# Kernel tuning notes

Hardware: AMD Instinct MI355X
Metric: run time of the kernel (lower is better)

## Reference

```python
import jax, jax.numpy as jnp
import numpy as np

LOG2PI = float(np.log(2.0 * np.pi))


def setup_inputs() -> dict:
    key = jax.random.key(0)
    ks = jax.random.split(key, 5)
    B, T, XD, C = 128, 2050, 6, 64
    return {
        "x": jax.random.normal(ks[0], (B, T, XD), jnp.float32),
        "observation_means": jax.random.uniform(ks[1], (C, XD), dtype=jnp.float32),
        "observation_stddevs": jax.random.uniform(ks[2], (C, XD), dtype=jnp.float32),
        "log_A": jax.random.normal(ks[3], (C, C), jnp.float32),
        "log_pi": jax.random.normal(ks[4], (C,), jnp.float32),
    }


def _emission_logprob(x, means, stds):
    # Normal(means[:, :4], relu(stds[:, :4]) + 0.1).log_prob(x[:, :, :4]) summed over feat dim
    mu = means[:, :4]                       # (C,4)
    sigma = jax.nn.relu(stds[:, :4]) + 0.1  # (C,4)
    z = (x[:, :, None, :4] - mu) / sigma    # (B,T,C,4)
    return jnp.sum(-0.5 * z * z - jnp.log(sigma) - 0.5 * LOG2PI, axis=-1)  # (B,T,C)


def _forward_scalers(logp, log_A, log_pi):
    # scaled HMM forward pass; returns per-step log normalizers (T,B)
    a0 = logp[:, 0] + log_pi
    s0 = jax.nn.logsumexp(a0, axis=-1)
    a0n = a0 - s0[:, None]

    def step(a_prev, lp_t):
        a = lp_t + jax.nn.logsumexp(a_prev[:, :, None] + log_A[None], axis=1)
        s = jax.nn.logsumexp(a, axis=-1)
        return a - s[:, None], s

    _, s_rest = jax.lax.scan(step, a0n, jnp.swapaxes(logp[:, 1:], 0, 1))
    return jnp.concatenate([s0[None], s_rest], axis=0)  # (T,B)


def _viterbi(logp, log_A, log_pi):
    d0 = logp[:, 0] + log_pi  # (B,C)

    def step(d_prev, lp_t):
        scores = d_prev[:, :, None] + log_A[None]  # (B,C_prev,C_cur)
        psi_t = jnp.argmax(scores, axis=1)
        d = jnp.max(scores, axis=1) + lp_t
        return d, psi_t

    d_last, psi = jax.lax.scan(step, d0, jnp.swapaxes(logp[:, 1:], 0, 1))  # psi: (T-1,B,C)
    c_last = jnp.argmax(d_last, axis=-1)  # (B,)

    def back(c_next, psi_t):
        c_t = jnp.take_along_axis(psi_t, c_next[:, None], axis=1)[:, 0]
        return c_t, c_t

    _, cs = jax.lax.scan(back, c_last, psi, reverse=True)  # (T-1,B)
    c = jnp.concatenate([cs, c_last[None]], axis=0)  # (T,B)
    return jnp.swapaxes(c, 0, 1)  # (B,T)


def reference(x, observation_means, observation_stddevs, log_A, log_pi):
    logA = jax.nn.log_softmax(log_A, axis=1)
    logpi = jax.nn.log_softmax(log_pi, axis=0)
    logp = _emission_logprob(x, observation_means, observation_stddevs)  # (B,T,C)
    scalers = _forward_scalers(logp, logA, logpi)                         # (T,B)
    logp_x = jnp.sum(scalers, axis=0)                                     # (B,)
    c_est = _viterbi(logp, logA, logpi)                                   # (B,T) int
    return logp_x, c_est
```

## Files before the change

### kernel.cpp

```cpp
#include <hip/hip_runtime.h>

#define T_LEN 2050
#define B_SZ 128
#define NCHUNK 33
#define HL2PI 0.91893853320467274178f

__device__ __forceinline__ float waveMax(float v) {
#pragma unroll
    for (int off = 32; off >= 1; off >>= 1)
        v = fmaxf(v, __shfl_xor(v, off, 64));
    return v;
}
__device__ __forceinline__ float waveSum(float v) {
#pragma unroll
    for (int off = 32; off >= 1; off >>= 1)
        v += __shfl_xor(v, off, 64);
    return v;
}
__device__ __forceinline__ void waveArgmax(float& v, int& idx) {
#pragma unroll
    for (int off = 32; off >= 1; off >>= 1) {
        float ov = __shfl_xor(v, off, 64);
        int   oi = __shfl_xor(idx, off, 64);
        if (ov > v || (ov == v && oi < idx)) { v = ov; idx = oi; }
    }
}
__device__ __forceinline__ void cfence() { asm volatile("" ::: "memory"); }

__device__ __forceinline__ float dppSumAll(float v) {
#define SSTEP(ctrl) { int t_ = __builtin_amdgcn_update_dpp(0, __float_as_int(v), ctrl, 0xf, 0xf, true); \
                      v = v + __int_as_float(t_); }
    SSTEP(0x111) SSTEP(0x112) SSTEP(0x114) SSTEP(0x118) SSTEP(0x142) SSTEP(0x143)
#undef SSTEP
    return __int_as_float(__builtin_amdgcn_readlane(__float_as_int(v), 63));
}
__device__ __forceinline__ float dppMaxAll(float v) {
#define MSTEP(ctrl) { int t_ = __builtin_amdgcn_update_dpp(__float_as_int(v), __float_as_int(v), ctrl, 0xf, 0xf, false); \
                      v = fmaxf(v, __int_as_float(t_)); }
    MSTEP(0x111) MSTEP(0x112) MSTEP(0x114) MSTEP(0x118) MSTEP(0x142) MSTEP(0x143)
#undef MSTEP
    return __int_as_float(__builtin_amdgcn_readlane(__float_as_int(v), 63));
}
__device__ __forceinline__ float rlane(int bits, int lane) {
    return __int_as_float(__builtin_amdgcn_readlane(bits, lane));
}

extern "C" __global__ __launch_bounds__(64, 1)
void hmm_prep(const float* __restrict__ logA_in,
              const float* __restrict__ logpi_in,
              float* __restrict__ lAg,
              float* __restrict__ lpig)
{
    __shared__ float la[64 * 65];
    __shared__ float rowlse[64];
    const int j = threadIdx.x;
#pragma unroll
    for (int k = 0; k < 64; ++k)
        la[k * 65 + j] = logA_in[k * 64 + j];
    cfence();
    {
        float m = -1e30f;
#pragma unroll
        for (int k = 0; k < 64; ++k) m = fmaxf(m, la[j * 65 + k]);
        float s = 0.f;
#pragma unroll
        for (int k = 0; k < 64; ++k) s += expf(la[j * 65 + k] - m);
        rowlse[j] = m + logf(s);
    }
    cfence();
    {
        float v = logpi_in[j];
        float m = waveMax(v);
        float s = waveSum(expf(v - m));
        lpig[j] = v - (m + logf(s));
    }
    float4* o = (float4*)lAg;
#pragma unroll
    for (int k = 0; k < 16; ++k) {
        float4 v;
        v.x = la[(4 * k + 0) * 65 + j] - rowlse[4 * k + 0];
        v.y = la[(4 * k + 1) * 65 + j] - rowlse[4 * k + 1];
        v.z = la[(4 * k + 2) * 65 + j] - rowlse[4 * k + 2];
        v.w = la[(4 * k + 3) * 65 + j] - rowlse[4 * k + 3];
        o[j * 16 + k] = v;
    }
}

extern "C" __global__ __launch_bounds__(256)
void hmm_emis(const float* __restrict__ x,
              const float* __restrict__ means,
              const float* __restrict__ stds,
              float* __restrict__ buf)
{
    const int wid = blockIdx.x * 4 + (threadIdx.x >> 6);
    const int j = threadIdx.x & 63;
    const int t = wid >> 7;
    const int b = wid & 127;

    const float* xt = x + ((size_t)b * T_LEN + t) * 6;
    float x0 = xt[0], x1 = xt[1], x2 = xt[2], x3 = xt[3];

    float mu0 = means[j * 6 + 0], mu1 = means[j * 6 + 1];
    float mu2 = means[j * 6 + 2], mu3 = means[j * 6 + 3];
    float sg0 = fmaxf(stds[j * 6 + 0], 0.f) + 0.1f;
    float sg1 = fmaxf(stds[j * 6 + 1], 0.f) + 0.1f;
    float sg2 = fmaxf(stds[j * 6 + 2], 0.f) + 0.1f;
    float sg3 = fmaxf(stds[j * 6 + 3], 0.f) + 0.1f;
    float ls0 = logf(sg0), ls1 = logf(sg1), ls2 = logf(sg2), ls3 = logf(sg3);

    float z0 = (x0 - mu0) / sg0, z1 = (x1 - mu1) / sg1;
    float z2 = (x2 - mu2) / sg2, z3 = (x3 - mu3) / sg3;
    float e0 = ((-0.5f * z0) * z0 - ls0) - HL2PI;
    float e1 = ((-0.5f * z1) * z1 - ls1) - HL2PI;
    float e2 = ((-0.5f * z2) * z2 - ls2) - HL2PI;
    float e3 = ((-0.5f * z3) * z3 - ls3) - HL2PI;
    float lp = ((e0 + e1) + e2) + e3;

    buf[((size_t)b * T_LEN + t) * 64 + j] = lp;
}

extern "C" __global__ __launch_bounds__(64, 1)
void hmm_main(const float* __restrict__ x,
              const float* __restrict__ means,
              const float* __restrict__ stds,
              const float* __restrict__ lAg,
              const float* __restrict__ lpig,
              float* __restrict__ out,
              float* __restrict__ buf,
              int* __restrict__ c_last)
{
    __shared__ __align__(16) float xs[12304];

    const int j   = threadIdx.x;
    const int bid = blockIdx.x;
    const bool is_fwd = (bid < B_SZ);
    const int b = is_fwd ? bid : bid - B_SZ;

    float lpi = lpig[j];

    if (is_fwd) {
        {
            const float4* xg4 = (const float4*)(x + (size_t)b * T_LEN * 6);
            float4* xs4 = (float4*)xs;
            for (int i = j; i < 3075; i += 64) xs4[i] = xg4[i];
        }
        float mu0 = means[j * 6 + 0], mu1 = means[j * 6 + 1];
        float mu2 = means[j * 6 + 2], mu3 = means[j * 6 + 3];
        float sg0 = fmaxf(stds[j * 6 + 0], 0.f) + 0.1f;
        float sg1 = fmaxf(stds[j * 6 + 1], 0.f) + 0.1f;
        float sg2 = fmaxf(stds[j * 6 + 2], 0.f) + 0.1f;
        float sg3 = fmaxf(stds[j * 6 + 3], 0.f) + 0.1f;
        float ls0 = logf(sg0), ls1 = logf(sg1), ls2 = logf(sg2), ls3 = logf(sg3);
        float i0 = 1.f / sg0, i1 = 1.f / sg1, i2 = 1.f / sg2, i3 = 1.f / sg3;
        float cst = -(ls0 + ls1 + ls2 + ls3) - 4.f * HL2PI;

        float Ac[64];
        {
            const float4* g = (const float4*)lAg;
#pragma unroll
            for (int k = 0; k < 16; ++k) {
                float4 v = g[j * 16 + k];
                Ac[4 * k + 0] = __expf(v.x); Ac[4 * k + 1] = __expf(v.y);
                Ac[4 * k + 2] = __expf(v.z); Ac[4 * k + 3] = __expf(v.w);
            }
        }
        cfence();

        float z0 = (xs[0] - mu0) * i0, z1 = (xs[1] - mu1) * i1;
        float z2 = (xs[2] - mu2) * i2, z3 = (xs[3] - mu3) * i3;
        float a0 = (cst - 0.5f * (z0 * z0 + z1 * z1 + z2 * z2 + z3 * z3)) + lpi;
        float m0a = dppMaxAll(a0);
        float u = __expf(a0 - m0a);
        float s0 = dppSumAll(u);
        double acc = (double)(m0a + __logf(s0));
        u *= (1.0f / s0);

        float mm_c, e_c;
        {
            float y0 = (xs[6] - mu0) * i0, y1 = (xs[7] - mu1) * i1;
            float y2 = (xs[8] - mu2) * i2, y3 = (xs[9] - mu3) * i3;
            float lp1 = cst - 0.5f * (y0 * y0 + y1 * y1 + y2 * y2 + y3 * y3);
            mm_c = dppMaxAll(lp1);
            e_c  = __expf(lp1 - mm_c);
        }

#pragma unroll 1
        for (int t = 1; t < T_LEN; ++t) {
            int o = ((t + 1 < T_LEN) ? (t + 1) : t) * 6;
            float y0 = xs[o], y1 = xs[o + 1], y2 = xs[o + 2], y3 = xs[o + 3];

            int ub = __float_as_int(u);
            float q0 = 0.f, q1 = 0.f, q2 = 0.f, q3 = 0.f;
#pragma unroll
            for (int k = 0; k < 16; ++k) {
                q0 = fmaf(rlane(ub, 4 * k + 0), Ac[4 * k + 0], q0);
                q1 = fmaf(rlane(ub, 4 * k + 1), Ac[4 * k + 1], q1);
                q2 = fmaf(rlane(ub, 4 * k + 2), Ac[4 * k + 2], q2);
                q3 = fmaf(rlane(ub, 4 * k + 3), Ac[4 * k + 3], q3);
            }
            float q = (q0 + q1) + (q2 + q3);
            u = q * e_c;
            acc += (double)mm_c;
            if ((t & 3) == 0) {
                float ss = dppSumAll(u);
                acc += (double)__logf(ss);
                u *= (1.0f / ss);
            }

            float w0 = (y0 - mu0) * i0, w1 = (y1 - mu1) * i1;
            float w2 = (y2 - mu2) * i2, w3 = (y3 - mu3) * i3;
            float lpn = cst - 0.5f * (w0 * w0 + w1 * w1 + w2 * w2 + w3 * w3);
            float mmn = dppMaxAll(lpn);
            e_c  = __expf(lpn - mmn);
            mm_c = mmn;
        }
        float sf = dppSumAll(u);
        acc += (double)__logf(sf);
        if (j == 0) out[b] = (float)acc;
    } else {
        float lA[64];
        {
            const float4* g = (const float4*)lAg;
#pragma unroll
            for (int k = 0; k < 16; ++k) {
                float4 v = g[j * 16 + k];
                lA[4 * k + 0] = v.x; lA[4 * k + 1] = v.y;
                lA[4 * k + 2] = v.z; lA[4 * k + 3] = v.w;
            }
        }
        float* bb = buf + (size_t)b * T_LEN * 64 + j;

        float dn = bb[0] + lpi;
        float l0 = bb[64], l1 = bb[128], l2 = bb[192], l3 = bb[256];
        bb[0] = dn;

#pragma unroll 1
        for (int t = 1; t < T_LEN; ++t) {
            float lp_c = l0; l0 = l1; l1 = l2; l2 = l3;
            int tp = t + 4; if (tp > T_LEN - 1) tp = T_LEN - 1;
            l3 = bb[(size_t)tp * 64];

            int db = __float_as_int(dn);
            float m0 = -3.4e38f, m1 = -3.4e38f, m2 = -3.4e38f, m3 = -3.4e38f;
#pragma unroll
            for (int k = 0; k < 8; ++k) {
                float t0 = rlane(db, 8 * k + 0) + lA[8 * k + 0];
                float t1 = rlane(db, 8 * k + 1) + lA[8 * k + 1];
                float t2 = rlane(db, 8 * k + 2) + lA[8 * k + 2];
                float t3 = rlane(db, 8 * k + 3) + lA[8 * k + 3];
                float t4 = rlane(db, 8 * k + 4) + lA[8 * k + 4];
                float t5 = rlane(db, 8 * k + 5) + lA[8 * k + 5];
                float t6 = rlane(db, 8 * k + 6) + lA[8 * k + 6];
                float t7 = rlane(db, 8 * k + 7) + lA[8 * k + 7];
                m0 = fmaxf(fmaxf(m0, t0), t1);
                m1 = fmaxf(fmaxf(m1, t2), t3);
                m2 = fmaxf(fmaxf(m2, t4), t5);
                m3 = fmaxf(fmaxf(m3, t6), t7);
            }
            float best = fmaxf(fmaxf(m0, m1), fmaxf(m2, m3));
            dn = best + lp_c;
            bb[(size_t)t * 64] = dn;
        }

        float vv = dn; int idx = j;
        waveArgmax(vv, idx);
        if (j == 0) c_last[b] = idx;
    }
}

extern "C" __global__ __launch_bounds__(256)
void hmm_psi(const float* __restrict__ buf,
             const float* __restrict__ lAg,
             unsigned char* __restrict__ psi)
{
    __shared__ __align__(16) float sd[4][64];
    const int warp = threadIdx.x >> 6;
    const int j = threadIdx.x & 63;
    const int wid = blockIdx.x * 4 + warp;

    float lA[64];
    {
        const float4* g = (const float4*)lAg;
#pragma unroll
        for (int k = 0; k < 16; ++k) {
            float4 v = g[j * 16 + k];
            lA[4 * k + 0] = v.x; lA[4 * k + 1] = v.y;
            lA[4 * k + 2] = v.z; lA[4 * k + 3] = v.w;
        }
    }
    const float4* dv = (const float4*)sd[warp];
    const int NP = 2049 * B_SZ;

    for (int p = wid; p < NP; p += 8192) {
        const int t = (p >> 7) + 1;
        const int b = p & 127;
        float dval = buf[((size_t)b * T_LEN + (t - 1)) * 64 + j];
        sd[warp][j] = dval;

        float bv0 = -3.4e38f, bv1 = -3.4e38f, bv2 = -3.4e38f, bv3 = -3.4e38f;
        int bi0 = 0, bi1 = 1, bi2 = 2, bi3 = 3;
#pragma unroll
        for (int k = 0; k < 16; ++k) {
            float4 dd = dv[k];
            float v0 = dd.x + lA[4 * k + 0];
            float v1 = dd.y + lA[4 * k + 1];
            float v2 = dd.z + lA[4 * k + 2];
            float v3 = dd.w + lA[4 * k + 3];
            if (v0 > bv0) { bv0 = v0; bi0 = 4 * k + 0; }
            if (v1 > bv1) { bv1 = v1; bi1 = 4 * k + 1; }
            if (v2 > bv2) { bv2 = v2; bi2 = 4 * k + 2; }
            if (v3 > bv3) { bv3 = v3; bi3 = 4 * k + 3; }
        }
        float best = bv0; int bidx = bi0;
        if (bv1 > best || (bv1 == best && bi1 < bidx)) { best = bv1; bidx = bi1; }
        if (bv2 > best || (bv2 == best && bi2 < bidx)) { best = bv2; bidx = bi2; }
        if (bv3 > best || (bv3 == best && bi3 < bidx)) { best = bv3; bidx = bi3; }

        psi[((size_t)t * B_SZ + b) * 64 + j] = (unsigned char)bidx;
    }
}

extern "C" __global__ __launch_bounds__(256)
void hmm_compose(const unsigned char* __restrict__ psi,
                 unsigned char* __restrict__ mt)
{
    const int w = blockIdx.x * 4 + (threadIdx.x >> 6);
    const int j = threadIdx.x & 63;
    const int g = w % NCHUNK;
    const int b = w / NCHUNK;
    const int e = (g < NCHUNK - 1) ? g * 64 + 64 : (T_LEN - 1);
    int M = j;
    for (int t = e; t >= g * 64 + 1; --t)
        M = psi[((size_t)t * B_SZ + b) * 64 + M];
    mt[((size_t)g * B_SZ + b) * 64 + j] = (unsigned char)M;
}

extern "C" __global__ __launch_bounds__(64, 1)
void hmm_fill(const unsigned char* __restrict__ psi,
              const unsigned char* __restrict__ mt,
              const int* __restrict__ c_last,
              float* __restrict__ out)
{
    __shared__ int sb[NCHUNK];
    const int b = blockIdx.x;
    const int g = threadIdx.x;
    const int cl = c_last[b];
    if (g == 0) {
        int cur = cl;
        for (int q = NCHUNK - 1; q >= 0; --q) {
            cur = mt[((size_t)q * B_SZ + b) * 64 + cur];
            sb[q] = cur;
        }
    }
    cfence();
    float* oc = out + B_SZ + (size_t)b * T_LEN;
    if (g == NCHUNK) {
        oc[T_LEN - 1] = (float)cl;
    } else if (g < NCHUNK) {
        const int e = (g < NCHUNK - 1) ? g * 64 + 64 : (T_LEN - 1);
        int s = (g < NCHUNK - 1) ? sb[g + 1] : cl;
        for (int t = e; t >= g * 64 + 1; --t) {
            s = psi[((size_t)t * B_SZ + b) * 64 + s];
            oc[t - 1] = (float)s;
        }
    }
}

extern "C" void kernel_launch(void* const* d_in, const int* in_sizes, int n_in,
                              void* d_out, int out_size, void* d_ws, size_t ws_size,
                              hipStream_t stream)
{
    const float* x      = (const float*)d_in[0];
    const float* means  = (const float*)d_in[1];
    const float* stds   = (const float*)d_in[2];
    const float* logA   = (const float*)d_in[3];
    const float* logpi  = (const float*)d_in[4];
    float* out = (float*)d_out;

    char* base = (char*)d_ws;
    float*         buf  = (float*)base;
    unsigned char* psi  = (unsigned char*)(base + 67174400);
    unsigned char* mt   = (unsigned char*)(base + 83968000);
    int*           cl   = (int*)(base + 84238336);
    float*         lAg  = (float*)(base + 84238848);
    float*         lpig = (float*)(base + 84255232);

    hipLaunchKernelGGL(hmm_prep, dim3(1), dim3(64), 0, stream, logA, logpi, lAg, lpig);
    hipLaunchKernelGGL(hmm_emis, dim3((T_LEN * B_SZ) / 4), dim3(256), 0, stream,
                       x, means, stds, buf);
    hipLaunchKernelGGL(hmm_main, dim3(2 * B_SZ), dim3(64), 0, stream,
                       x, means, stds, lAg, lpig, out, buf, cl);
    hipLaunchKernelGGL(hmm_psi, dim3(2048), dim3(256), 0, stream, buf, lAg, psi);
    hipLaunchKernelGGL(hmm_compose, dim3((NCHUNK * B_SZ) / 4), dim3(256), 0, stream, psi, mt);
    hipLaunchKernelGGL(hmm_fill, dim3(B_SZ), dim3(64), 0, stream, psi, mt, cl, out);
}
```

Before: 1.059 ms.

## Process two batch sequences per wavefront in forward and Viterbi recurrences

Each hmm_main block now handles two batch elements, interleaving their independent recurrences so the lane-broadcast/FMA or max chains of one sequence can hide the latency of the other. The grid halves from 256 to 128 single-wave blocks, and shared memory doubles to hold both x sequences. This trades per-wave ILP for fewer concurrent waves and higher register pressure, on a GPU with far more CUs than blocks.

```diff
diff --git a/kernel.cpp b/kernel.cpp
--- a/kernel.cpp
+++ b/kernel.cpp
@@ -129,20 +129,23 @@
               float* __restrict__ buf,
               int* __restrict__ c_last)
 {
-    __shared__ __align__(16) float xs[12304];
+    __shared__ __align__(16) float xs[2 * 12304];
 
     const int j   = threadIdx.x;
     const int bid = blockIdx.x;
-    const bool is_fwd = (bid < B_SZ);
-    const int b = is_fwd ? bid : bid - B_SZ;
+    const bool is_fwd = (bid < 64);
+    const int p = is_fwd ? bid : bid - 64;
+    const int b0 = 2 * p, b1 = 2 * p + 1;
 
     float lpi = lpig[j];
 
     if (is_fwd) {
         {
-            const float4* xg4 = (const float4*)(x + (size_t)b * T_LEN * 6);
-            float4* xs4 = (float4*)xs;
-            for (int i = j; i < 3075; i += 64) xs4[i] = xg4[i];
+            const float4* xg0 = (const float4*)(x + (size_t)b0 * T_LEN * 6);
+            const float4* xg1 = (const float4*)(x + (size_t)b1 * T_LEN * 6);
+            float4* xs0 = (float4*)xs;
+            float4* xs1 = (float4*)(xs + 12304);
+            for (int i = j; i < 3075; i += 64) { xs0[i] = xg0[i]; xs1[i] = xg1[i]; }
         }
         float mu0 = means[j * 6 + 0], mu1 = means[j * 6 + 1];
         float mu2 = means[j * 6 + 2], mu3 = means[j * 6 + 3];
@@ -166,57 +169,85 @@
         }
         cfence();
 
-        float z0 = (xs[0] - mu0) * i0, z1 = (xs[1] - mu1) * i1;
-        float z2 = (xs[2] - mu2) * i2, z3 = (xs[3] - mu3) * i3;
-        float a0 = (cst - 0.5f * (z0 * z0 + z1 * z1 + z2 * z2 + z3 * z3)) + lpi;
-        float m0a = dppMaxAll(a0);
-        float u = __expf(a0 - m0a);
-        float s0 = dppSumAll(u);
-        double acc = (double)(m0a + __logf(s0));
-        u *= (1.0f / s0);
-
-        float mm_c, e_c;
-        {
-            float y0 = (xs[6] - mu0) * i0, y1 = (xs[7] - mu1) * i1;
-            float y2 = (xs[8] - mu2) * i2, y3 = (xs[9] - mu3) * i3;
-            float lp1 = cst - 0.5f * (y0 * y0 + y1 * y1 + y2 * y2 + y3 * y3);
-            mm_c = dppMaxAll(lp1);
-            e_c  = __expf(lp1 - mm_c);
+        const float* X0 = xs;
+        const float* X1 = xs + 12304;
+
+        float u0, u1; double acc0, acc1;
+        {
+            float a = (cst - 0.5f * (((X0[0]-mu0)*i0)*((X0[0]-mu0)*i0) + ((X0[1]-mu1)*i1)*((X0[1]-mu1)*i1)
+                                   + ((X0[2]-mu2)*i2)*((X0[2]-mu2)*i2) + ((X0[3]-mu3)*i3)*((X0[3]-mu3)*i3))) + lpi;
+            float m = dppMaxAll(a);
+            u0 = __expf(a - m);
+            float s = dppSumAll(u0);
+            acc0 = (double)(m + __logf(s));
+            u0 *= (1.0f / s);
+        }
+        {
+            float a = (cst - 0.5f * (((X1[0]-mu0)*i0)*((X1[0]-mu0)*i0) + ((X1[1]-mu1)*i1)*((X1[1]-mu1)*i1)
+                                   + ((X1[2]-mu2)*i2)*((X1[2]-mu2)*i2) + ((X1[3]-mu3)*i3)*((X1[3]-mu3)*i3))) + lpi;
+            float m = dppMaxAll(a);
+            u1 = __expf(a - m);
+            float s = dppSumAll(u1);
+            acc1 = (double)(m + __logf(s));
+            u1 *= (1.0f / s);
+        }
+
+        float mm_c0, e_c0, mm_c1, e_c1;
+        {
+            float w0 = (X0[6]-mu0)*i0, w1 = (X0[7]-mu1)*i1, w2 = (X0[8]-mu2)*i2, w3 = (X0[9]-mu3)*i3;
+            float lp = cst - 0.5f * (w0*w0 + w1*w1 + w2*w2 + w3*w3);
+            mm_c0 = dppMaxAll(lp); e_c0 = __expf(lp - mm_c0);
+            float v0 = (X1[6]-mu0)*i0, v1 = (X1[7]-mu1)*i1, v2 = (X1[8]-mu2)*i2, v3 = (X1[9]-mu3)*i3;
+            float lq = cst - 0.5f * (v0*v0 + v1*v1 + v2*v2 + v3*v3);
+            mm_c1 = dppMaxAll(lq); e_c1 = __expf(lq - mm_c1);
         }
 
 #pragma unroll 1
         for (int t = 1; t < T_LEN; ++t) {
             int o = ((t + 1 < T_LEN) ? (t + 1) : t) * 6;
-            float y0 = xs[o], y1 = xs[o + 1], y2 = xs[o + 2], y3 = xs[o + 3];
-
-            int ub = __float_as_int(u);
-            float q0 = 0.f, q1 = 0.f, q2 = 0.f, q3 = 0.f;
+            float y00 = X0[o], y01 = X0[o+1], y02 = X0[o+2], y03 = X0[o+3];
+            float y10 = X1[o], y11 = X1[o+1], y12 = X1[o+2], y13 = X1[o+3];
+
+            int ub0 = __float_as_int(u0);
+            int ub1 = __float_as_int(u1);
+            float qa0 = 0.f, qa1 = 0.f, qa2 = 0.f, qa3 = 0.f;
+            float qb0 = 0.f, qb1 = 0.f, qb2 = 0.f, qb3 = 0.f;
 #pragma unroll
             for (int k = 0; k < 16; ++k) {
-                q0 = fmaf(rlane(ub, 4 * k + 0), Ac[4 * k + 0], q0);
-                q1 = fmaf(rlane(ub, 4 * k + 1), Ac[4 * k + 1], q1);
-                q2 = fmaf(rlane(ub, 4 * k + 2), Ac[4 * k + 2], q2);
-                q3 = fmaf(rlane(ub, 4 * k + 3), Ac[4 * k + 3], q3);
+                qa0 = fmaf(rlane(ub0, 4*k+0), Ac[4*k+0], qa0);
+                qb0 = fmaf(rlane(ub1, 4*k+0), Ac[4*k+0], qb0);
+                qa1 = fmaf(rlane(ub0, 4*k+1), Ac[4*k+1], qa1);
+                qb1 = fmaf(rlane(ub1, 4*k+1), Ac[4*k+1], qb1);
+                qa2 = fmaf(rlane(ub0, 4*k+2), Ac[4*k+2], qa2);
+                qb2 = fmaf(rlane(ub1, 4*k+2), Ac[4*k+2], qb2);
+                qa3 = fmaf(rlane(ub0, 4*k+3), Ac[4*k+3], qa3);
+                qb3 = fmaf(rlane(ub1, 4*k+3), Ac[4*k+3], qb3);
             }
-            float q = (q0 + q1) + (q2 + q3);
-            u = q * e_c;
-            acc += (double)mm_c;
+            u0 = ((qa0 + qa1) + (qa2 + qa3)) * e_c0;
+            u1 = ((qb0 + qb1) + (qb2 + qb3)) * e_c1;
+            acc0 += (double)mm_c0;
+            acc1 += (double)mm_c1;
             if ((t & 3) == 0) {
-                float ss = dppSumAll(u);
-                acc += (double)__logf(ss);
-                u *= (1.0f / ss);
+                float s0 = dppSumAll(u0);
+                float s1 = dppSumAll(u1);
+                acc0 += (double)__logf(s0); u0 *= (1.0f / s0);
+                acc1 += (double)__logf(s1); u1 *= (1.0f / s1);
             }
 
-            float w0 = (y0 - mu0) * i0, w1 = (y1 - mu1) * i1;
-            float w2 = (y2 - mu2) * i2, w3 = (y3 - mu3) * i3;
-            float lpn = cst - 0.5f * (w0 * w0 + w1 * w1 + w2 * w2 + w3 * w3);
-            float mmn = dppMaxAll(lpn);
-            e_c  = __expf(lpn - mmn);
-            mm_c = mmn;
-        }
-        float sf = dppSumAll(u);
-        acc += (double)__logf(sf);
-        if (j == 0) out[b] = (float)acc;
+            float w0 = (y00-mu0)*i0, w1 = (y01-mu1)*i1, w2 = (y02-mu2)*i2, w3 = (y03-mu3)*i3;
+            float lp = cst - 0.5f * (w0*w0 + w1*w1 + w2*w2 + w3*w3);
+            float v0 = (y10-mu0)*i0, v1 = (y11-mu1)*i1, v2 = (y12-mu2)*i2, v3 = (y13-mu3)*i3;
+            float lq = cst - 0.5f * (v0*v0 + v1*v1 + v2*v2 + v3*v3);
+            float mn0 = dppMaxAll(lp);
+            float mn1 = dppMaxAll(lq);
+            e_c0 = __expf(lp - mn0); mm_c0 = mn0;
+            e_c1 = __expf(lq - mn1); mm_c1 = mn1;
+        }
+        float sf0 = dppSumAll(u0);
+        float sf1 = dppSumAll(u1);
+        acc0 += (double)__logf(sf0);
+        acc1 += (double)__logf(sf1);
+        if (j == 0) { out[b0] = (float)acc0; out[b1] = (float)acc1; }
     } else {
         float lA[64];
         {
@@ -228,43 +259,53 @@
                 lA[4 * k + 2] = v.z; lA[4 * k + 3] = v.w;
             }
         }
-        float* bb = buf + (size_t)b * T_LEN * 64 + j;
-
-        float dn = bb[0] + lpi;
-        float l0 = bb[64], l1 = bb[128], l2 = bb[192], l3 = bb[256];
-        bb[0] = dn;
+        float* bb0 = buf + (size_t)b0 * T_LEN * 64 + j;
+        float* bb1 = buf + (size_t)b1 * T_LEN * 64 + j;
+
+        float dn0 = bb0[0] + lpi;
+        float dn1 = bb1[0] + lpi;
+        float a0 = bb0[64], a1 = bb0[128], a2 = bb0[192], a3 = bb0[256];
+        float c0 = bb1[64], c1 = bb1[128], c2 = bb1[192], c3 = bb1[256];
+        bb0[0] = dn0; bb1[0] = dn1;
 
 #pragma unroll 1
         for (int t = 1; t < T_LEN; ++t) {
-            float lp_c = l0; l0 = l1; l1 = l2; l2 = l3;
+            float lp0 = a0; a0 = a1; a1 = a2; a2 = a3;
+            float lp1 = c0; c0 = c1; c1 = c2; c2 = c3;
             int tp = t + 4; if (tp > T_LEN - 1) tp = T_LEN - 1;
-            l3 = bb[(size_t)tp * 64];
-
-            int db = __float_as_int(dn);
-            float m0 = -3.4e38f, m1 = -3.4e38f, m2 = -3.4e38f, m3 = -3.4e38f;
-#pragma unroll
-            for (int k = 0; k < 8; ++k) {
-                float t0 = rlane(db, 8 * k + 0) + lA[8 * k + 0];
-                float t1 = rlane(db, 8 * k + 1) + lA[8 * k + 1];
-                float t2 = rlane(db, 8 * k + 2) + lA[8 * k + 2];
-                float t3 = rlane(db, 8 * k + 3) + lA[8 * k + 3];
-                float t4 = rlane(db, 8 * k + 4) + lA[8 * k + 4];
-                float t5 = rlane(db, 8 * k + 5) + lA[8 * k + 5];
-                float t6 = rlane(db, 8 * k + 6) + lA[8 * k + 6];
-                float t7 = rlane(db, 8 * k + 7) + lA[8 * k + 7];
-                m0 = fmaxf(fmaxf(m0, t0), t1);
-                m1 = fmaxf(fmaxf(m1, t2), t3);
-                m2 = fmaxf(fmaxf(m2, t4), t5);
-                m3 = fmaxf(fmaxf(m3, t6), t7);
+            a3 = bb0[(size_t)tp * 64];
+            c3 = bb1[(size_t)tp * 64];
+
+            int db0 = __float_as_int(dn0);
+            int db1 = __float_as_int(dn1);
+            float m00 = -3.4e38f, m01 = -3.4e38f, m02 = -3.4e38f, m03 = -3.4e38f;
+            float m10 = -3.4e38f, m11 = -3.4e38f, m12 = -3.4e38f, m13 = -3.4e38f;
+#pragma unroll
+            for (int k = 0; k < 16; ++k) {
+                float t00 = rlane(db0, 4*k+0) + lA[4*k+0];
+                float t10 = rlane(db1, 4*k+0) + lA[4*k+0];
+                float t01 = rlane(db0, 4*k+1) + lA[4*k+1];
+                float t11 = rlane(db1, 4*k+1) + lA[4*k+1];
+                float t02 = rlane(db0, 4*k+2) + lA[4*k+2];
+                float t12 = rlane(db1, 4*k+2) + lA[4*k+2];
+                float t03 = rlane(db0, 4*k+3) + lA[4*k+3];
+                float t13 = rlane(db1, 4*k+3) + lA[4*k+3];
+                m00 = fmaxf(m00, t00); m10 = fmaxf(m10, t10);
+                m01 = fmaxf(m01, t01); m11 = fmaxf(m11, t11);
+                m02 = fmaxf(m02, t02); m12 = fmaxf(m12, t12);
+                m03 = fmaxf(m03, t03); m13 = fmaxf(m13, t13);
             }
-            float best = fmaxf(fmaxf(m0, m1), fmaxf(m2, m3));
-            dn = best + lp_c;
-            bb[(size_t)t * 64] = dn;
-        }
-
-        float vv = dn; int idx = j;
-        waveArgmax(vv, idx);
-        if (j == 0) c_last[b] = idx;
+            dn0 = fmaxf(fmaxf(m00, m01), fmaxf(m02, m03)) + lp0;
+            dn1 = fmaxf(fmaxf(m10, m11), fmaxf(m12, m13)) + lp1;
+            bb0[(size_t)t * 64] = dn0;
+            bb1[(size_t)t * 64] = dn1;
+        }
+
+        float v0 = dn0; int i0x = j;
+        waveArgmax(v0, i0x);
+        float v1 = dn1; int i1x = j;
+        waveArgmax(v1, i1x);
+        if (j == 0) { c_last[b0] = i0x; c_last[b1] = i1x; }
     }
 }
 
@@ -388,7 +429,7 @@
     hipLaunchKernelGGL(hmm_prep, dim3(1), dim3(64), 0, stream, logA, logpi, lAg, lpig);
     hipLaunchKernelGGL(hmm_emis, dim3((T_LEN * B_SZ) / 4), dim3(256), 0, stream,
                        x, means, stds, buf);
-    hipLaunchKernelGGL(hmm_main, dim3(2 * B_SZ), dim3(64), 0, stream,
+    hipLaunchKernelGGL(hmm_main, dim3(B_SZ), dim3(64), 0, stream,
                        x, means, stds, lAg, lpig, out, buf, cl);
     hipLaunchKernelGGL(hmm_psi, dim3(2048), dim3(256), 0, stream, buf, lAg, psi);
     hipLaunchKernelGGL(hmm_compose, dim3((NCHUNK * B_SZ) / 4), dim3(256), 0, stream, psi, mt);
```

Result: slower. 2.256 ms (+113.0%).

## Broadcast recurrence state via LDS and precompute per-step emission maxima

Applied to the files above, without the earlier changes.

The forward and Viterbi recurrences stop broadcasting the 64-state vector with readlane. Each step now writes the vector to a small LDS buffer and reads it back as sixteen float4 loads. The emission kernel also computes a per-(b,t) wave max and stores it, so the forward loop no longer runs a DPP max reduction every step and instead prefetches that max from global memory. The cost is an LDS round trip on the serial dependency chain plus extra global writes and reads for the max array, which shares workspace space with the psi buffer written later.

```diff
diff --git a/kernel.cpp b/kernel.cpp
--- a/kernel.cpp
+++ b/kernel.cpp
@@ -40,9 +40,6 @@
     MSTEP(0x111) MSTEP(0x112) MSTEP(0x114) MSTEP(0x118) MSTEP(0x142) MSTEP(0x143)
 #undef MSTEP
     return __int_as_float(__builtin_amdgcn_readlane(__float_as_int(v), 63));
-}
-__device__ __forceinline__ float rlane(int bits, int lane) {
-    return __int_as_float(__builtin_amdgcn_readlane(bits, lane));
 }
 
 extern "C" __global__ __launch_bounds__(64, 1)
@@ -90,7 +87,8 @@
 void hmm_emis(const float* __restrict__ x,
               const float* __restrict__ means,
               const float* __restrict__ stds,
-              float* __restrict__ buf)
+              float* __restrict__ buf,
+              float* __restrict__ m_pre)
 {
     const int wid = blockIdx.x * 4 + (threadIdx.x >> 6);
     const int j = threadIdx.x & 63;
@@ -117,6 +115,8 @@
     float lp = ((e0 + e1) + e2) + e3;
 
     buf[((size_t)b * T_LEN + t) * 64 + j] = lp;
+    float mm = waveMax(lp);
+    if (j == 0) m_pre[(size_t)b * T_LEN + t] = mm;
 }
 
 extern "C" __global__ __launch_bounds__(64, 1)
@@ -127,9 +127,11 @@
               const float* __restrict__ lpig,
               float* __restrict__ out,
               float* __restrict__ buf,
+              const float* __restrict__ m_pre,
               int* __restrict__ c_last)
 {
     __shared__ __align__(16) float xs[12304];
+    __shared__ __align__(16) float pbuf[64];
 
     const int j   = threadIdx.x;
     const int bid = blockIdx.x;
@@ -137,6 +139,7 @@
     const int b = is_fwd ? bid : bid - B_SZ;
 
     float lpi = lpig[j];
+    const float4* pv = (const float4*)pbuf;
 
     if (is_fwd) {
         {
@@ -174,32 +177,37 @@
         float s0 = dppSumAll(u);
         double acc = (double)(m0a + __logf(s0));
         u *= (1.0f / s0);
-
-        float mm_c, e_c;
-        {
-            float y0 = (xs[6] - mu0) * i0, y1 = (xs[7] - mu1) * i1;
-            float y2 = (xs[8] - mu2) * i2, y3 = (xs[9] - mu3) * i3;
-            float lp1 = cst - 0.5f * (y0 * y0 + y1 * y1 + y2 * y2 + y3 * y3);
-            mm_c = dppMaxAll(lp1);
-            e_c  = __expf(lp1 - mm_c);
-        }
+        pbuf[j] = u;
+        float4 rr[16];
+#pragma unroll
+        for (int k = 0; k < 16; ++k) rr[k] = pv[k];
+
+        const float* mp = m_pre + (size_t)b * T_LEN;
+        float g0 = mp[1], g1 = mp[2], g2 = mp[3], g3 = mp[4];
 
 #pragma unroll 1
         for (int t = 1; t < T_LEN; ++t) {
-            int o = ((t + 1 < T_LEN) ? (t + 1) : t) * 6;
+            float mm_c = g0; g0 = g1; g1 = g2; g2 = g3;
+            int tp = t + 4; if (tp > T_LEN - 1) tp = T_LEN - 1;
+            g3 = mp[tp];
+
+            int o = t * 6;
             float y0 = xs[o], y1 = xs[o + 1], y2 = xs[o + 2], y3 = xs[o + 3];
-
-            int ub = __float_as_int(u);
+            float w0 = (y0 - mu0) * i0, w1 = (y1 - mu1) * i1;
+            float w2 = (y2 - mu2) * i2, w3 = (y3 - mu3) * i3;
+            float lp = cst - 0.5f * (w0 * w0 + w1 * w1 + w2 * w2 + w3 * w3);
+            float e_c = __expf(lp - mm_c);
+
             float q0 = 0.f, q1 = 0.f, q2 = 0.f, q3 = 0.f;
 #pragma unroll
             for (int k = 0; k < 16; ++k) {
-                q0 = fmaf(rlane(ub, 4 * k + 0), Ac[4 * k + 0], q0);
-                q1 = fmaf(rlane(ub, 4 * k + 1), Ac[4 * k + 1], q1);
-                q2 = fmaf(rlane(ub, 4 * k + 2), Ac[4 * k + 2], q2);
-                q3 = fmaf(rlane(ub, 4 * k + 3), Ac[4 * k + 3], q3);
+                float4 pp = rr[k];
+                q0 = fmaf(pp.x, Ac[4 * k + 0], q0);
+                q1 = fmaf(pp.y, Ac[4 * k + 1], q1);
+                q2 = fmaf(pp.z, Ac[4 * k + 2], q2);
+                q3 = fmaf(pp.w, Ac[4 * k + 3], q3);
             }
-            float q = (q0 + q1) + (q2 + q3);
-            u = q * e_c;
+            u = ((q0 + q1) + (q2 + q3)) * e_c;
             acc += (double)mm_c;
             if ((t & 3) == 0) {
                 float ss = dppSumAll(u);
@@ -207,12 +215,9 @@
                 u *= (1.0f / ss);
             }
 
-            float w0 = (y0 - mu0) * i0, w1 = (y1 - mu1) * i1;
-            float w2 = (y2 - mu2) * i2, w3 = (y3 - mu3) * i3;
-            float lpn = cst - 0.5f * (w0 * w0 + w1 * w1 + w2 * w2 + w3 * w3);
-            float mmn = dppMaxAll(lpn);
-            e_c  = __expf(lpn - mmn);
-            mm_c = mmn;
+            pbuf[j] = u;
+#pragma unroll
+            for (int k = 0; k < 16; ++k) rr[k] = pv[k];
         }
         float sf = dppSumAll(u);
         acc += (double)__logf(sf);
@@ -233,6 +238,10 @@
         float dn = bb[0] + lpi;
         float l0 = bb[64], l1 = bb[128], l2 = bb[192], l3 = bb[256];
         bb[0] = dn;
+        pbuf[j] = dn;
+        float4 rr[16];
+#pragma unroll
+        for (int k = 0; k < 16; ++k) rr[k] = pv[k];
 
 #pragma unroll 1
         for (int t = 1; t < T_LEN; ++t) {
@@ -240,26 +249,21 @@
             int tp = t + 4; if (tp > T_LEN - 1) tp = T_LEN - 1;
             l3 = bb[(size_t)tp * 64];
 
-            int db = __float_as_int(dn);
             float m0 = -3.4e38f, m1 = -3.4e38f, m2 = -3.4e38f, m3 = -3.4e38f;
 #pragma unroll
-            for (int k = 0; k < 8; ++k) {
-                float t0 = rlane(db, 8 * k + 0) + lA[8 * k + 0];
-                float t1 = rlane(db, 8 * k + 1) + lA[8 * k + 1];
-                float t2 = rlane(db, 8 * k + 2) + lA[8 * k + 2];
-                float t3 = rlane(db, 8 * k + 3) + lA[8 * k + 3];
-                float t4 = rlane(db, 8 * k + 4) + lA[8 * k + 4];
-                float t5 = rlane(db, 8 * k + 5) + lA[8 * k + 5];
-                float t6 = rlane(db, 8 * k + 6) + lA[8 * k + 6];
-                float t7 = rlane(db, 8 * k + 7) + lA[8 * k + 7];
-                m0 = fmaxf(fmaxf(m0, t0), t1);
-                m1 = fmaxf(fmaxf(m1, t2), t3);
-                m2 = fmaxf(fmaxf(m2, t4), t5);
-                m3 = fmaxf(fmaxf(m3, t6), t7);
+            for (int k = 0; k < 16; ++k) {
+                float4 dd = rr[k];
+                m0 = fmaxf(m0, dd.x + lA[4 * k + 0]);
+                m1 = fmaxf(m1, dd.y + lA[4 * k + 1]);
+                m2 = fmaxf(m2, dd.z + lA[4 * k + 2]);
+                m3 = fmaxf(m3, dd.w + lA[4 * k + 3]);
             }
-            float best = fmaxf(fmaxf(m0, m1), fmaxf(m2, m3));
-            dn = best + lp_c;
+            dn = fmaxf(fmaxf(m0, m1), fmaxf(m2, m3)) + lp_c;
+
             bb[(size_t)t * 64] = dn;
+            pbuf[j] = dn;
+#pragma unroll
+            for (int k = 0; k < 16; ++k) rr[k] = pv[k];
         }
 
         float vv = dn; int idx = j;
@@ -378,18 +382,19 @@
     float* out = (float*)d_out;
 
     char* base = (char*)d_ws;
-    float*         buf  = (float*)base;
-    unsigned char* psi  = (unsigned char*)(base + 67174400);
-    unsigned char* mt   = (unsigned char*)(base + 83968000);
-    int*           cl   = (int*)(base + 84238336);
-    float*         lAg  = (float*)(base + 84238848);
-    float*         lpig = (float*)(base + 84255232);
+    float*         buf   = (float*)base;
+    unsigned char* psi   = (unsigned char*)(base + 67174400);
+    float*         m_pre = (float*)(base + 67174400);
+    unsigned char* mt    = (unsigned char*)(base + 83968000);
+    int*           cl    = (int*)(base + 84238336);
+    float*         lAg   = (float*)(base + 84238848);
+    float*         lpig  = (float*)(base + 84255232);
 
     hipLaunchKernelGGL(hmm_prep, dim3(1), dim3(64), 0, stream, logA, logpi, lAg, lpig);
     hipLaunchKernelGGL(hmm_emis, dim3((T_LEN * B_SZ) / 4), dim3(256), 0, stream,
-                       x, means, stds, buf);
+                       x, means, stds, buf, m_pre);
     hipLaunchKernelGGL(hmm_main, dim3(2 * B_SZ), dim3(64), 0, stream,
-                       x, means, stds, lAg, lpig, out, buf, cl);
+                       x, means, stds, lAg, lpig, out, buf, m_pre, cl);
     hipLaunchKernelGGL(hmm_psi, dim3(2048), dim3(256), 0, stream, buf, lAg, psi);
     hipLaunchKernelGGL(hmm_compose, dim3((NCHUNK * B_SZ) / 4), dim3(256), 0, stream, psi, mt);
     hipLaunchKernelGGL(hmm_fill, dim3(B_SZ), dim3(64), 0, stream, psi, mt, cl, out);
```

Result: no change. 1.056 ms (-0.3%).
